# Kernel optimization log

Hardware: AMD Instinct MI355X
Metric: run time of the kernel (lower is better)

Reference implementation:

```python
import jax, jax.numpy as jnp
import numpy as np

D = 128; H = 8; L = 3; FF = 512; HID = 512
B = 512; N = 20
KD = D // H
CLIP = 10.0


def _bn(x, g, b):
    # BatchNorm1d over flattened (B*n, D), training-mode batch stats, affine
    m = jnp.mean(x, axis=(0, 1)); v = jnp.var(x, axis=(0, 1))
    return (x - m) * jax.lax.rsqrt(v + 1e-5) * g + b


def _mha(x, Wq, Wk, Wv, Wo):
    q = jnp.einsum('bnd,hdk->hbnk', x, Wq)
    k = jnp.einsum('bnd,hdk->hbnk', x, Wk)
    v = jnp.einsum('bnd,hdk->hbnk', x, Wv)
    a = jax.nn.softmax(jnp.einsum('hbnk,hbmk->hbnm', q, k) / np.float32(np.sqrt(KD)), axis=-1)
    h = jnp.einsum('hbnm,hbmk->hbnk', a, v)
    return jnp.einsum('hbnk,hkd->bnd', h, Wo)


def _encode(x, Wq, Wk, Wv, Wo, g1, b1, fW1, fb1, fW2, fb2, g2, b2):
    for l in range(L):
        x = _bn(x + _mha(x, Wq[l], Wk[l], Wv[l], Wo[l]), g1[l], b1[l])
        f = jnp.maximum(x @ fW1[l] + fb1[l], 0.0) @ fW2[l] + fb2[l]
        x = _bn(x + f, g2[l], b2[l])
    return x


def _forward(coords, Wi, bi, W_ph, enc_Wq, enc_Wk, enc_Wv, enc_Wo, enc_g1, enc_b1,
             enc_ffW1, enc_ffb1, enc_ffW2, enc_ffb2, enc_g2, enc_b2,
             W_node, W_fixed, W_step, W_out, Wc1, bc1, Wc2, bc2):
    Bs, Ns, _ = coords.shape
    bid = jnp.arange(Bs)
    x = coords @ Wi + bi                                   # (B,N,D) initial embeddings
    crd = coords
    node_idx = jnp.broadcast_to(jnp.arange(Ns)[None, :], (Bs, Ns))
    # state is re-made each step, so step context is always the placeholder
    step_ctx = jnp.broadcast_to(W_ph[None, :], (Bs, 2 * D))
    ctx_q = step_ctx @ W_step                              # (B,D), constant across steps
    log_ps = []; irs = []; vals = []; tours = []
    first = prev = cur = None
    for i in range(Ns):  # sequential decode loop (shapes shrink each step)
        n = Ns - i
        E = _encode(x, enc_Wq, enc_Wk, enc_Wv, enc_Wo, enc_g1, enc_b1,
                    enc_ffW1, enc_ffb1, enc_ffW2, enc_ffb2, enc_g2, enc_b2)  # (B,n,D)
        g_mean = jnp.mean(E, axis=1)                       # (B,D)
        q = g_mean @ W_fixed + ctx_q                       # (B,D)
        gK, gV, lK = jnp.split(E @ W_node, 3, axis=-1)     # each (B,n,D)
        qh = q.reshape(Bs, H, KD)
        a = jax.nn.softmax(jnp.einsum('bhk,bnhk->bhn', qh, gK.reshape(Bs, n, H, KD)) / np.float32(np.sqrt(KD)), axis=-1)
        glimpse = jnp.einsum('bhn,bnhk->bhk', a, gV.reshape(Bs, n, H, KD)).reshape(Bs, D) @ W_out
        logits = jnp.tanh(jnp.einsum('bd,bnd->bn', glimpse, lK) / np.float32(np.sqrt(D))) * CLIP
        log_p = jax.nn.log_softmax(logits, axis=-1)        # mask all-False (fresh state)
        sel = jnp.argmax(log_p, axis=1)                    # greedy decode
        log_ps.append(log_p[bid, sel])
        cur = crd[bid, sel]
        if i == 0:
            first = cur
            irs.append(jnp.zeros((Bs,), coords.dtype))
        else:
            irs.append(-jnp.sqrt(jnp.sum((cur - prev) ** 2, axis=1)))
        h = jnp.maximum(jnp.concatenate([g_mean, step_ctx], axis=1) @ Wc1 + bc1, 0.0)
        vals.append((h @ Wc2 + bc2)[:, 0])
        tours.append(node_idx[bid, sel])
        if i < Ns - 1:
            sel_mask = (jnp.arange(n)[None, :] == sel[:, None]).astype(jnp.int32)
            keep = jnp.argsort(sel_mask, axis=1)[:, : n - 1]  # stable: drops selected, keeps order
            crd = jnp.take_along_axis(crd, keep[:, :, None], axis=1)
            x = jnp.take_along_axis(x, keep[:, :, None], axis=1)
            node_idx = jnp.take_along_axis(node_idx, keep, axis=1)
        prev = cur
    reward_final = -jnp.sqrt(jnp.sum((first - cur) ** 2, axis=1))
    tours = jnp.stack(tours, axis=1)                        # (B,N) int
    d = jnp.take_along_axis(coords, tours[:, :, None], axis=1)
    cost = jnp.sum(jnp.linalg.norm(d[:, 1:] - d[:, :-1], axis=2), axis=1) + jnp.linalg.norm(d[:, 0] - d[:, -1], axis=1)
    return (jnp.stack(log_ps, 1), jnp.stack(irs, 1), jnp.stack(vals, 1), cost, reward_final, tours)


def setup_inputs():
    key = jax.random.key(0)
    ks = jax.random.split(key, 16)
    def nrm(k, shp, scale=0.02):
        return jax.random.normal(k, shp, dtype=jnp.float32) * scale
    return {
        'coords': jax.random.uniform(ks[0], (B, N, 2), dtype=jnp.float32),
        'Wi': nrm(ks[1], (2, D), 0.5),
        'bi': jnp.zeros((D,), jnp.float32),
        'W_ph': jax.random.uniform(ks[2], (2 * D,), jnp.float32, -1.0, 1.0),
        'enc_Wq': nrm(ks[3], (L, H, D, KD)),
        'enc_Wk': nrm(ks[4], (L, H, D, KD)),
        'enc_Wv': nrm(ks[5], (L, H, D, KD)),
        'enc_Wo': nrm(ks[6], (L, H, KD, D)),
        'enc_g1': jnp.ones((L, D), jnp.float32),
        'enc_b1': jnp.zeros((L, D), jnp.float32),
        'enc_ffW1': nrm(ks[7], (L, D, FF)),
        'enc_ffb1': jnp.zeros((L, FF), jnp.float32),
        'enc_ffW2': nrm(ks[8], (L, FF, D)),
        'enc_ffb2': jnp.zeros((L, D), jnp.float32),
        'enc_g2': jnp.ones((L, D), jnp.float32),
        'enc_b2': jnp.zeros((L, D), jnp.float32),
        'W_node': nrm(ks[9], (D, 3 * D)),
        'W_fixed': nrm(ks[10], (D, D)),
        'W_step': nrm(ks[11], (2 * D, D)),
        'W_out': nrm(ks[12], (D, D)),
        'Wc1': nrm(ks[13], (3 * D, HID)),
        'bc1': jnp.zeros((HID,), jnp.float32),
        'Wc2': nrm(ks[14], (HID, 1)),
        'bc2': jnp.zeros((1,), jnp.float32),
    }


def reference(coords, Wi, bi, W_ph, enc_Wq, enc_Wk, enc_Wv, enc_Wo, enc_g1, enc_b1,
              enc_ffW1, enc_ffb1, enc_ffW2, enc_ffb2, enc_g2, enc_b2,
              W_node, W_fixed, W_step, W_out, Wc1, bc1, Wc2, bc2):
    return _forward(coords, Wi, bi, W_ph, enc_Wq, enc_Wk, enc_Wv, enc_Wo, enc_g1, enc_b1,
                    enc_ffW1, enc_ffb1, enc_ffW2, enc_ffb2, enc_g2, enc_b2,
                    W_node, W_fixed, W_step, W_out, Wc1, bc1, Wc2, bc2)
```

## Files before the change

kernel.cpp:

```cpp
#include <hip/hip_runtime.h>
#include <cmath>

namespace {
constexpr int Hc = 8, FFc = 512, HIDc = 512;
}

struct Params {
  const float *coords, *Wi, *bi, *W_ph;
  const float *Wq, *Wk, *Wv, *Wo, *g1, *b1, *fW1, *fb1, *fW2, *fb2, *g2, *b2;
  const float *W_node, *W_fixed, *W_step, *W_out, *Wc1, *bc1, *Wc2, *bc2;
  float* out;
};

__device__ __align__(16) float g_bn[120 * 8 * 256];
__device__ __align__(16) float g_x[512 * 2560];
__device__ __align__(16) float g_t[512 * 2560];
__device__ __align__(16) float g_crd[512 * 40];
__device__ int   g_idx[512 * 20];
__device__ float g_state[512 * 8];
__device__ __align__(16) float g_ctxq[128];
__device__ __align__(16) float g_cctx[512];
__device__ __align__(16) float g_Wqp[3 * 16384];
__device__ __align__(16) float g_Wkp[3 * 16384];
__device__ __align__(16) float g_Wvp[3 * 16384];
__device__ __align__(16) float g_Wop[3 * 16384];
__device__ __align__(16) float g_W1q[3 * 65536];
__device__ __align__(16) float g_W2q[3 * 65536];
__device__ __align__(16) float g_Wnp[49152];
__device__ __align__(16) float g_Wfp[16384];
__device__ __align__(16) float g_Woup[16384];
__device__ __align__(16) float g_Wc1p[65536];

#define DOT4(a, b) ((a).x*(b).x + (a).y*(b).y + (a).z*(b).z + (a).w*(b).w)

__device__ __forceinline__ void bn_coef(int slot, const float* g, const float* bb, float cnt,
                                        float* s_scale, float* s_shift, int tid) {
  if (tid < 128) {
    float sm = 0.f, sq = 0.f;
#pragma unroll
    for (int r = 0; r < 8; r++) {
      const float* s = &g_bn[(slot * 8 + r) * 256];
      sm += s[tid]; sq += s[128 + tid];
    }
    float m_ = sm / cnt;
    float v_ = sq / cnt - m_ * m_;
    float rs = rsqrtf(v_ + 1e-5f);
    float sc = rs * g[tid];
    s_scale[tid] = sc;
    s_shift[tid] = bb[tid] - m_ * sc;
  }
}

__global__ __launch_bounds__(256) void kinit(Params p) {
  const int tid = threadIdx.x, b = blockIdx.x;
  const int gid = b * 256 + tid, GS = 512 * 256;
  for (int i = gid; i < 120 * 8 * 256; i += GS) g_bn[i] = 0.f;
  for (int e = tid; e < 2560; e += 256) {
    int i = e >> 7, d = e & 127;
    float cx = p.coords[b * 40 + 2 * i], cy = p.coords[b * 40 + 2 * i + 1];
    g_x[b * 2560 + e] = cx * p.Wi[d] + cy * p.Wi[128 + d] + p.bi[d];
  }
  if (tid < 40) g_crd[b * 40 + tid] = p.coords[b * 40 + tid];
  if (tid < 20) g_idx[b * 20 + tid] = tid;
  if (tid < 8) g_state[b * 8 + tid] = 0.f;
  if (b == 0) {
    if (tid < 128) {
      float a = 0.f;
      for (int j = 0; j < 256; j++) a += p.W_ph[j] * p.W_step[j * 128 + tid];
      g_ctxq[tid] = a;
    }
    for (int jj = tid; jj < 512; jj += 256) {
      float a = p.bc1[jj];
      for (int e = 0; e < 256; e++) a += p.W_ph[e] * p.Wc1[(128 + e) * 512 + jj];
      g_cctx[jj] = a;
    }
  }
  for (int e = gid; e < 3 * 16384; e += GS) {
    int sub = e & 3, rest = e >> 2;
    int j = rest & 127, rest2 = rest >> 7, d4 = rest2 & 31, l = rest2 >> 5;
    int d = d4 * 4 + sub;
    int src = l * 16384 + (j >> 4) * 2048 + d * 16 + (j & 15);
    g_Wqp[e] = p.Wq[src]; g_Wkp[e] = p.Wk[src]; g_Wvp[e] = p.Wv[src];
    int c = d;
    g_Wop[e] = p.Wo[l * 16384 + (c >> 4) * 2048 + (c & 15) * 128 + j];
  }
  for (int e = gid; e < 3 * 65536; e += GS) {
    int sub = e & 3, f = (e >> 2) & 16383, l = e >> 16;
    int cg = f & 127, c = (f >> 7) & 3, k4 = f >> 9;
    g_W1q[e] = p.fW1[l * 65536 + (k4 * 4 + sub) * 512 + cg * 4 + c];
  }
  for (int e = gid; e < 3 * 65536; e += GS) {
    int sub = e & 3, f = (e >> 2) & 16383, l = e >> 16;
    int j = f & 127, k4 = f >> 7;
    g_W2q[e] = p.fW2[l * 65536 + (k4 * 4 + sub) * 128 + j];
  }
  for (int e = gid; e < 49152; e += GS) {
    int sub = e & 3, rest = e >> 2;
    int col = rest % 384, e4 = rest / 384;
    g_Wnp[e] = p.W_node[(e4 * 4 + sub) * 384 + col];
  }
  for (int e = gid; e < 16384; e += GS) {
    int sub = e & 3, rest = e >> 2;
    int j = rest & 127, e4 = rest >> 7;
    g_Wfp[e] = p.W_fixed[(e4 * 4 + sub) * 128 + j];
    g_Woup[e] = p.W_out[(e4 * 4 + sub) * 128 + j];
  }
  for (int e = gid; e < 65536; e += GS) {
    int sub = e & 3, rest = e >> 2;
    int jj = rest & 511, e4 = rest >> 9;
    g_Wc1p[e] = p.Wc1[(e4 * 4 + sub) * 512 + jj];
  }
}

__global__ __launch_bounds__(512, 4) void ka(Params p, int step, int l) {
  const int tid = threadIdx.x, b = blockIdx.x;
  const int n = 20 - step;
  __shared__ __align__(16) float s_t[2560];
  __shared__ __align__(16) float s_q[2560];
  __shared__ float s_kT[2560];
  __shared__ __align__(16) float s_v[2560];
  __shared__ float s_att[3200];
  __shared__ __align__(16) float s_scale[128], s_shift[128];
  __shared__ float s_bnp[4 * 128 * 2];

  if (l > 0)
    bn_coef(step * 6 + (l - 1) * 2 + 1, p.g2 + (l - 1) * 128, p.b2 + (l - 1) * 128,
            (float)(512 * n), s_scale, s_shift, tid);
  __syncthreads();
  const float4* src4 = (const float4*)((l == 0 ? g_x : g_t) + b * 2560);
  float4* st4 = (float4*)s_t;
  for (int e4 = tid; e4 < n * 32; e4 += 512) {
    float4 x = src4[e4];
    if (l > 0) {
      float4 sc = ((const float4*)s_scale)[e4 & 31];
      float4 sh = ((const float4*)s_shift)[e4 & 31];
      x.x = x.x * sc.x + sh.x; x.y = x.y * sc.y + sh.y;
      x.z = x.z * sc.z + sh.z; x.w = x.w * sc.w + sh.w;
    }
    st4[e4] = x;
  }
  __syncthreads();
  {
    const int j = tid & 127, rg2 = tid >> 7;
    const float4* wq4 = (const float4*)g_Wqp + l * 4096 + j;
    const float4* wk4 = (const float4*)g_Wkp + l * 4096 + j;
    const float4* wv4 = (const float4*)g_Wvp + l * 4096 + j;
    float aq[5], ak[5], av[5];
#pragma unroll
    for (int r = 0; r < 5; r++) { aq[r] = 0.f; ak[r] = 0.f; av[r] = 0.f; }
    float4 bq = wq4[0], bk = wk4[0], bv = wv4[0];
#pragma unroll 2
    for (int d4 = 0; d4 < 32; d4++) {
      const int dn = (d4 + 1) & 31;
      float4 nq = wq4[dn * 128], nk = wk4[dn * 128], nv = wv4[dn * 128];
#pragma unroll
      for (int r = 0; r < 5; r++) {
        int i = rg2 + 4 * r;
        if (i < n) {
          float4 x = st4[i * 32 + d4];
          aq[r] += DOT4(x, bq); ak[r] += DOT4(x, bk); av[r] += DOT4(x, bv);
        }
      }
      bq = nq; bk = nk; bv = nv;
    }
#pragma unroll
    for (int r = 0; r < 5; r++) {
      int i = rg2 + 4 * r;
      if (i < n) {
        s_q[i * 128 + j] = aq[r];
        s_kT[j * 20 + i] = ak[r];
        s_v[i * 128 + j] = av[r];
      }
    }
  }
  __syncthreads();
  const int nn = n * n;
  for (int e = tid; e < 8 * nn; e += 512) {
    int hl = e / nn, rem = e % nn, i = rem / n, m = rem % n;
    float dacc = 0.f;
#pragma unroll
    for (int k2 = 0; k2 < 16; k2++)
      dacc += s_q[i * 128 + hl * 16 + k2] * s_kT[(hl * 16 + k2) * 20 + m];
    s_att[hl * 400 + i * 20 + m] = dacc * 0.25f;
  }
  __syncthreads();
  for (int r = tid; r < 8 * n; r += 512) {
    int hl = r / n, i = r % n;
    float* row = s_att + hl * 400 + i * 20;
    float mx = row[0];
    for (int m = 1; m < n; m++) mx = fmaxf(mx, row[m]);
    float s = 0.f;
    for (int m = 0; m < n; m++) { float ev = __expf(row[m] - mx); row[m] = ev; s += ev; }
    float inv = 1.f / s;
    for (int m = 0; m < n; m++) row[m] *= inv;
  }
  __syncthreads();
  for (int e = tid; e < 8 * n * 16; e += 512) {
    int hl = e / (n * 16), rem = e % (n * 16), i = rem >> 4, k2 = rem & 15;
    const float* arow = s_att + hl * 400 + i * 20;
    float acc = 0.f;
    for (int m = 0; m < n; m++) acc += arow[m] * s_v[m * 128 + hl * 16 + k2];
    s_q[i * 128 + hl * 16 + k2] = acc;
  }
  __syncthreads();
  {
    const int j2 = tid & 127, rh2 = tid >> 7;
    const int s = rh2 & 1, rhalf = rh2 >> 1;
    const float4* sh4 = (const float4*)s_q;
    float acc[5];
#pragma unroll
    for (int r = 0; r < 5; r++) {
      int i = s + 2 * (rhalf + 2 * r);
      acc[r] = (i < n) ? s_t[i * 128 + j2] : 0.f;
    }
    const float4* wo4 = (const float4*)g_Wop + l * 4096 + j2;
    float4 wb0 = wo4[0], wb1 = wo4[128];
#pragma unroll 2
    for (int c4 = 0; c4 < 32; c4++) {
      float4 wn = wo4[((c4 + 2) & 31) * 128];
#pragma unroll
      for (int r = 0; r < 5; r++) {
        int i = s + 2 * (rhalf + 2 * r);
        if (i < n) { float4 h = sh4[i * 32 + c4]; acc[r] += DOT4(h, wb0); }
      }
      wb0 = wb1; wb1 = wn;
    }
    float sm = 0.f, sq = 0.f;
#pragma unroll
    for (int r = 0; r < 5; r++) {
      int i = s + 2 * (rhalf + 2 * r);
      if (i < n) { g_t[b * 2560 + i * 128 + j2] = acc[r]; sm += acc[r]; sq += acc[r] * acc[r]; }
    }
    s_bnp[(rh2 * 128 + j2) * 2] = sm;
    s_bnp[(rh2 * 128 + j2) * 2 + 1] = sq;
  }
  __syncthreads();
  if (tid < 128) {
    float sm = 0.f, sq = 0.f;
#pragma unroll
    for (int h = 0; h < 4; h++) { sm += s_bnp[(h * 128 + tid) * 2]; sq += s_bnp[(h * 128 + tid) * 2 + 1]; }
    float* slot = &g_bn[((step * 6 + l * 2) * 8 + (b & 7)) * 256];
    atomicAdd(&slot[tid], sm);
    atomicAdd(&slot[128 + tid], sq);
  }
}

__global__ __launch_bounds__(256, 4) void kff(Params p, int step, int l) {
  const int tid = threadIdx.x, bx = blockIdx.x;
  const int n = 20 - step;
  const int r0 = bx * 16;
  const int wid = tid >> 6, lam = tid & 63;
  const int g = wid >> 1, rh = wid & 1;
  __shared__ __align__(16) float s_x[16 * 128];
  __shared__ __align__(16) float s_hid[16 * 512];
  __shared__ __align__(16) float s_scale[128], s_shift[128];
  __shared__ float s_bn[8 * 128 * 2];

  bn_coef(step * 6 + l * 2, p.g1 + l * 128, p.b1 + l * 128, (float)(512 * n), s_scale, s_shift, tid);
  __syncthreads();
  {
    float4* sx4 = (float4*)s_x;
    for (int e4 = tid; e4 < 16 * 32; e4 += 256) {
      int row = e4 >> 5, d4 = e4 & 31;
      int r = r0 + row, b = r / n, i = r - b * n;
      float4 x = *(const float4*)(g_t + b * 2560 + i * 128 + d4 * 4);
      float4 sc = ((const float4*)s_scale)[d4];
      float4 sf = ((const float4*)s_shift)[d4];
      x.x = x.x * sc.x + sf.x; x.y = x.y * sc.y + sf.y;
      x.z = x.z * sc.z + sf.z; x.w = x.w * sc.w + sf.w;
      sx4[e4] = x;
    }
  }
  __syncthreads();
  {
    const int cg = g * 64 + lam;
    float acc[8][4];
#pragma unroll
    for (int rr = 0; rr < 8; rr++)
#pragma unroll
      for (int c = 0; c < 4; c++) acc[rr][c] = 0.f;
    const float4* w1 = (const float4*)g_W1q + l * 16384 + cg;
    const float4* xx = (const float4*)s_x + rh * 8 * 32;
    float4 wb[4];
#pragma unroll
    for (int c = 0; c < 4; c++) wb[c] = w1[c * 128];
#pragma unroll 2
    for (int k4 = 0; k4 < 32; k4++) {
      float4 wn[4];
      const int kn = (k4 + 1) & 31;
#pragma unroll
      for (int c = 0; c < 4; c++) wn[c] = w1[kn * 512 + c * 128];
#pragma unroll
      for (int rr = 0; rr < 8; rr++) {
        float4 xr = xx[rr * 32 + k4];
#pragma unroll
        for (int c = 0; c < 4; c++) acc[rr][c] += DOT4(xr, wb[c]);
      }
#pragma unroll
      for (int c = 0; c < 4; c++) wb[c] = wn[c];
    }
    float4 b1v = *(const float4*)(p.fb1 + l * FFc + cg * 4);
#pragma unroll
    for (int rr = 0; rr < 8; rr++) {
      int row = rh * 8 + rr;
      float4 u;
      u.x = fmaxf(acc[rr][0] + b1v.x, 0.f); u.y = fmaxf(acc[rr][1] + b1v.y, 0.f);
      u.z = fmaxf(acc[rr][2] + b1v.z, 0.f); u.w = fmaxf(acc[rr][3] + b1v.w, 0.f);
      *(float4*)&s_hid[row * 512 + cg * 4] = u;
    }
  }
  __syncthreads();
  {
    const int j = g * 64 + lam;
    float acc[8];
#pragma unroll
    for (int rr = 0; rr < 8; rr++) acc[rr] = 0.f;
    const float4* w2 = (const float4*)g_W2q + l * 16384 + j;
    const float4* hh = (const float4*)s_hid + rh * 8 * 128;
    float4 wb0 = w2[0], wb1 = w2[128];
#pragma unroll 2
    for (int k4 = 0; k4 < 128; k4++) {
      float4 wn = w2[((k4 + 2) & 127) * 128];
#pragma unroll
      for (int rr = 0; rr < 8; rr++) acc[rr] += DOT4(hh[rr * 128 + k4], wb0);
      wb0 = wb1; wb1 = wn;
    }
    const float f2 = p.fb2[l * 128 + j];
    float u[8];
#pragma unroll
    for (int rr = 0; rr < 8; rr++) {
      int row = rh * 8 + rr;
      int r = r0 + row, b = r / n, i = r - b * n;
      u[rr] = s_x[row * 128 + j] + acc[rr] + f2;
      g_t[b * 2560 + i * 128 + j] = u[rr];
    }
#pragma unroll
    for (int q = 0; q < 4; q++) {
      const int sb = ((rh * 4 + q) * 128 + j) * 2;
      s_bn[sb] = u[2 * q] + u[2 * q + 1];
      s_bn[sb + 1] = u[2 * q] * u[2 * q] + u[2 * q + 1] * u[2 * q + 1];
    }
  }
  __syncthreads();
  if (tid < 128) {
    float sm = 0.f, sq = 0.f;
#pragma unroll
    for (int rg = 0; rg < 8; rg++) { sm += s_bn[(rg * 128 + tid) * 2]; sq += s_bn[(rg * 128 + tid) * 2 + 1]; }
    float* slot = &g_bn[((step * 6 + l * 2 + 1) * 8 + (bx & 7)) * 256];
    atomicAdd(&slot[tid], sm);
    atomicAdd(&slot[128 + tid], sq);
  }
}

__global__ __launch_bounds__(512, 4) void kd(Params p, int step) {
  const int tid = threadIdx.x, b = blockIdx.x;
  const int n = 20 - step;
  __shared__ __align__(16) float s_t[2560];
  __shared__ __align__(16) float s_dec[7680];
  __shared__ __align__(16) float s_scale[128], s_shift[128];
  __shared__ __align__(16) float s_gmean[128];
  __shared__ float s_red[512];
  __shared__ float s_qv[128], s_glq[128];
  __shared__ __align__(16) float s_gl[128];
  __shared__ float s_att[160];
  __shared__ float s_logits[20];
  __shared__ int s_sel;

  bn_coef(step * 6 + 5, p.g2 + 2 * 128, p.b2 + 2 * 128, (float)(512 * n), s_scale, s_shift, tid);
  __syncthreads();
  const float4* src4 = (const float4*)(g_t + b * 2560);
  float4* st4 = (float4*)s_t;
  for (int e4 = tid; e4 < n * 32; e4 += 512) {
    float4 x = src4[e4];
    float4 sc = ((const float4*)s_scale)[e4 & 31];
    float4 sf = ((const float4*)s_shift)[e4 & 31];
    x.x = x.x * sc.x + sf.x; x.y = x.y * sc.y + sf.y;
    x.z = x.z * sc.z + sf.z; x.w = x.w * sc.w + sf.w;
    st4[e4] = x;
  }
  __syncthreads();
  if (tid < 128) {
    float ssum = 0.f;
    for (int i2 = 0; i2 < n; i2++) ssum += s_t[i2 * 128 + tid];
    s_gmean[tid] = ssum / (float)n;
  }
  __syncthreads();
  {
    const int cb = tid & 63, rg = tid >> 6;
    float acc[6][3];
#pragma unroll
    for (int cc = 0; cc < 6; cc++)
#pragma unroll
      for (int r = 0; r < 3; r++) acc[cc][r] = 0.f;
    const float4* wn4 = (const float4*)g_Wnp + cb;
    float4 wb[6];
#pragma unroll
    for (int cc = 0; cc < 6; cc++) wb[cc] = wn4[cc * 64];
#pragma unroll 2
    for (int d4 = 0; d4 < 32; d4++) {
      const int dn = (d4 + 1) & 31;
      float4 wn[6];
#pragma unroll
      for (int cc = 0; cc < 6; cc++) wn[cc] = wn4[dn * 384 + cc * 64];
#pragma unroll
      for (int r = 0; r < 3; r++) {
        int i = rg + 8 * r;
        if (i < n) {
          float4 x = st4[i * 32 + d4];
#pragma unroll
          for (int cc = 0; cc < 6; cc++) acc[cc][r] += DOT4(x, wb[cc]);
        }
      }
#pragma unroll
      for (int cc = 0; cc < 6; cc++) wb[cc] = wn[cc];
    }
#pragma unroll
    for (int r = 0; r < 3; r++) {
      int i = rg + 8 * r;
      if (i < n) {
#pragma unroll
        for (int cc = 0; cc < 6; cc++)
          s_dec[i * 384 + cb + 64 * cc] = acc[cc][r];
      }
    }
  }
  {
    const int jj = tid;
    float a = g_cctx[jj];
    const float4* wc4 = (const float4*)g_Wc1p + jj;
    const float4* gm4 = (const float4*)s_gmean;
    float4 wb0 = wc4[0], wb1 = wc4[512];
#pragma unroll 2
    for (int e4 = 0; e4 < 32; e4++) {
      float4 wn = wc4[((e4 + 2) & 31) * 512];
      float4 g = gm4[e4]; a += DOT4(g, wb0);
      wb0 = wb1; wb1 = wn;
    }
    s_red[tid] = fmaxf(a, 0.f) * p.Wc2[jj];
  }
  if (tid < 128) {
    float a = g_ctxq[tid];
    const float4* wf4 = (const float4*)g_Wfp + tid;
    const float4* gm4 = (const float4*)s_gmean;
    float4 wb0 = wf4[0], wb1 = wf4[128];
#pragma unroll 2
    for (int e4 = 0; e4 < 32; e4++) {
      float4 wn = wf4[((e4 + 2) & 31) * 128];
      float4 g = gm4[e4]; a += DOT4(g, wb0);
      wb0 = wb1; wb1 = wn;
    }
    s_qv[tid] = a;
  }
  __syncthreads();
#pragma unroll
  for (int sred = 256; sred > 0; sred >>= 1) {
    if (tid < sred) s_red[tid] += s_red[tid + sred];
    __syncthreads();
  }
  for (int e = tid; e < Hc * n; e += 512) {
    int hh = e / n, m = e % n;
    float dacc = 0.f;
#pragma unroll
    for (int k2 = 0; k2 < 16; k2++) dacc += s_qv[hh * 16 + k2] * s_dec[m * 384 + hh * 16 + k2];
    s_att[hh * 20 + m] = dacc * 0.25f;
  }
  __syncthreads();
  if (tid < Hc) {
    float* row = s_att + tid * 20;
    float mx = row[0];
    for (int m = 1; m < n; m++) mx = fmaxf(mx, row[m]);
    float s = 0.f;
    for (int m = 0; m < n; m++) { float ev = __expf(row[m] - mx); row[m] = ev; s += ev; }
    float inv = 1.f / s;
    for (int m = 0; m < n; m++) row[m] *= inv;
  }
  __syncthreads();
  if (tid < 128) {
    int hh = tid >> 4;
    const float* arow = s_att + hh * 20;
    float acc = 0.f;
    for (int m = 0; m < n; m++) acc += arow[m] * s_dec[m * 384 + 128 + tid];
    s_gl[tid] = acc;
  }
  __syncthreads();
  if (tid < 128) {
    float a = 0.f;
    const float4* wo4 = (const float4*)g_Woup + tid;
    const float4* rr4 = (const float4*)s_gl;
    float4 wb0 = wo4[0], wb1 = wo4[128];
#pragma unroll 2
    for (int c4 = 0; c4 < 32; c4++) {
      float4 wn = wo4[((c4 + 2) & 31) * 128];
      float4 r = rr4[c4]; a += DOT4(r, wb0);
      wb0 = wb1; wb1 = wn;
    }
    s_glq[tid] = a;
  }
  __syncthreads();
  if (tid < n) {
    const float* lk = s_dec + tid * 384 + 256;
    float dacc = 0.f;
    for (int d = 0; d < 128; d++) dacc += s_glq[d] * lk[d];
    s_logits[tid] = 10.f * tanhf(dacc / 11.313708498984761f);
  }
  __syncthreads();
  if (tid == 0) {
    float mx = s_logits[0]; int sel = 0;
    for (int i2 = 1; i2 < n; i2++) if (s_logits[i2] > mx) { mx = s_logits[i2]; sel = i2; }
    float s = 0.f;
    for (int i2 = 0; i2 < n; i2++) s += __expf(s_logits[i2] - mx);
    p.out[b * 20 + step] = -logf(s);
    float cx = g_crd[b * 40 + 2 * sel], cy = g_crd[b * 40 + 2 * sel + 1];
    float ir = 0.f;
    if (step > 0) {
      float dx = cx - g_state[b * 8 + 0], dy = cy - g_state[b * 8 + 1];
      float dist = sqrtf(dx * dx + dy * dy);
      ir = -dist;
      g_state[b * 8 + 4] += dist;
    } else { g_state[b * 8 + 2] = cx; g_state[b * 8 + 3] = cy; g_state[b * 8 + 4] = 0.f; }
    p.out[10240 + b * 20 + step] = ir;
    p.out[31744 + b * 20 + step] = (float)g_idx[b * 20 + sel];
    g_state[b * 8 + 0] = cx; g_state[b * 8 + 1] = cy;
    if (step == 19) {
      float dx = g_state[b * 8 + 2] - cx, dy = g_state[b * 8 + 3] - cy;
      float dc = sqrtf(dx * dx + dy * dy);
      p.out[31232 + b] = -dc;
      p.out[30720 + b] = g_state[b * 8 + 4] + dc;
    }
    p.out[20480 + b * 20 + step] = s_red[0] + p.bc2[0];
    s_sel = sel;
  }
  __syncthreads();
  if (step < 19) {
    const int sel = s_sel;
    const int movecnt = (n - 1 - sel) * 128;
    float tmp[5]; float crdv = 0.f; int idxv = 0;
#pragma unroll
    for (int r = 0; r < 5; r++) { int e = tid + r * 512; if (e < movecnt) tmp[r] = g_x[b * 2560 + (sel + 1) * 128 + e]; }
    const int mc2 = (n - 1 - sel) * 2;
    if (tid < mc2) crdv = g_crd[b * 40 + (sel + 1) * 2 + tid];
    if (tid < n - 1 - sel) idxv = g_idx[b * 20 + sel + 1 + tid];
    __syncthreads();
#pragma unroll
    for (int r = 0; r < 5; r++) { int e = tid + r * 512; if (e < movecnt) g_x[b * 2560 + sel * 128 + e] = tmp[r]; }
    if (tid < mc2) g_crd[b * 40 + sel * 2 + tid] = crdv;
    if (tid < n - 1 - sel) g_idx[b * 20 + sel + tid] = idxv;
  }
}

extern "C" void kernel_launch(void* const* d_in, const int* in_sizes, int n_in,
                              void* d_out, int out_size, void* d_ws, size_t ws_size,
                              hipStream_t stream) {
  Params p;
  p.coords  = (const float*)d_in[0];
  p.Wi      = (const float*)d_in[1];
  p.bi      = (const float*)d_in[2];
  p.W_ph    = (const float*)d_in[3];
  p.Wq      = (const float*)d_in[4];
  p.Wk      = (const float*)d_in[5];
  p.Wv      = (const float*)d_in[6];
  p.Wo      = (const float*)d_in[7];
  p.g1      = (const float*)d_in[8];
  p.b1      = (const float*)d_in[9];
  p.fW1     = (const float*)d_in[10];
  p.fb1     = (const float*)d_in[11];
  p.fW2     = (const float*)d_in[12];
  p.fb2     = (const float*)d_in[13];
  p.g2      = (const float*)d_in[14];
  p.b2      = (const float*)d_in[15];
  p.W_node  = (const float*)d_in[16];
  p.W_fixed = (const float*)d_in[17];
  p.W_step  = (const float*)d_in[18];
  p.W_out   = (const float*)d_in[19];
  p.Wc1     = (const float*)d_in[20];
  p.bc1     = (const float*)d_in[21];
  p.Wc2     = (const float*)d_in[22];
  p.bc2     = (const float*)d_in[23];
  p.out = (float*)d_out;

  kinit<<<512, 256, 0, stream>>>(p);
  for (int step = 0; step < 20; step++) {
    const int n = 20 - step;
    for (int l = 0; l < 3; l++) {
      ka<<<512, 512, 0, stream>>>(p, step, l);
      kff<<<dim3(32 * n), 256, 0, stream>>>(p, step, l);
    }
    kd<<<512, 512, 0, stream>>>(p, step);
  }
}
```

Baseline: 5.679 ms.

## Rebalance thread-to-output mapping in attention QKV, FFN and decoder projections

After: 6.268 ms. 10.4% more time.

```diff
diff --git a/kernel.cpp b/kernel.cpp
--- a/kernel.cpp
+++ b/kernel.cpp
@@ -86,8 +86,8 @@
   }
   for (int e = gid; e < 3 * 65536; e += GS) {
     int sub = e & 3, f = (e >> 2) & 16383, l = e >> 16;
-    int cg = f & 127, c = (f >> 7) & 3, k4 = f >> 9;
-    g_W1q[e] = p.fW1[l * 65536 + (k4 * 4 + sub) * 512 + cg * 4 + c];
+    int cg = f & 255, c = (f >> 8) & 1, k4 = f >> 9;
+    g_W1q[e] = p.fW1[l * 65536 + (k4 * 4 + sub) * 512 + cg * 2 + c];
   }
   for (int e = gid; e < 3 * 65536; e += GS) {
     int sub = e & 3, f = (e >> 2) & 16383, l = e >> 16;
@@ -140,22 +140,22 @@
     st4[e4] = x;
   }
   __syncthreads();
-  {
-    const int j = tid & 127, rg2 = tid >> 7;
+  if (tid < 256) {
+    const int j = tid & 127, rg = tid >> 7;
     const float4* wq4 = (const float4*)g_Wqp + l * 4096 + j;
     const float4* wk4 = (const float4*)g_Wkp + l * 4096 + j;
     const float4* wv4 = (const float4*)g_Wvp + l * 4096 + j;
-    float aq[5], ak[5], av[5];
-#pragma unroll
-    for (int r = 0; r < 5; r++) { aq[r] = 0.f; ak[r] = 0.f; av[r] = 0.f; }
+    float aq[10], ak[10], av[10];
+#pragma unroll
+    for (int r = 0; r < 10; r++) { aq[r] = 0.f; ak[r] = 0.f; av[r] = 0.f; }
     float4 bq = wq4[0], bk = wk4[0], bv = wv4[0];
 #pragma unroll 2
     for (int d4 = 0; d4 < 32; d4++) {
       const int dn = (d4 + 1) & 31;
       float4 nq = wq4[dn * 128], nk = wk4[dn * 128], nv = wv4[dn * 128];
 #pragma unroll
-      for (int r = 0; r < 5; r++) {
-        int i = rg2 + 4 * r;
+      for (int r = 0; r < 10; r++) {
+        int i = rg + 2 * r;
         if (i < n) {
           float4 x = st4[i * 32 + d4];
           aq[r] += DOT4(x, bq); ak[r] += DOT4(x, bk); av[r] += DOT4(x, bv);
@@ -164,8 +164,8 @@
       bq = nq; bk = nk; bv = nv;
     }
 #pragma unroll
-    for (int r = 0; r < 5; r++) {
-      int i = rg2 + 4 * r;
+    for (int r = 0; r < 10; r++) {
+      int i = rg + 2 * r;
       if (i < n) {
         s_q[i * 128 + j] = aq[r];
         s_kT[j * 20 + i] = ak[r];
@@ -250,7 +250,6 @@
   const int n = 20 - step;
   const int r0 = bx * 16;
   const int wid = tid >> 6, lam = tid & 63;
-  const int g = wid >> 1, rh = wid & 1;
   __shared__ __align__(16) float s_x[16 * 128];
   __shared__ __align__(16) float s_hid[16 * 512];
   __shared__ __align__(16) float s_scale[128], s_shift[128];
@@ -273,72 +272,79 @@
   }
   __syncthreads();
   {
-    const int cg = g * 64 + lam;
-    float acc[8][4];
-#pragma unroll
-    for (int rr = 0; rr < 8; rr++)
-#pragma unroll
-      for (int c = 0; c < 4; c++) acc[rr][c] = 0.f;
+    const int cg = wid * 64 + lam;
+    float acc[16][2];
+#pragma unroll
+    for (int row = 0; row < 16; row++) { acc[row][0] = 0.f; acc[row][1] = 0.f; }
     const float4* w1 = (const float4*)g_W1q + l * 16384 + cg;
-    const float4* xx = (const float4*)s_x + rh * 8 * 32;
-    float4 wb[4];
-#pragma unroll
-    for (int c = 0; c < 4; c++) wb[c] = w1[c * 128];
+    const float4* xx = (const float4*)s_x;
+    float4 wb0 = w1[0], wb1 = w1[256];
 #pragma unroll 2
     for (int k4 = 0; k4 < 32; k4++) {
-      float4 wn[4];
       const int kn = (k4 + 1) & 31;
-#pragma unroll
-      for (int c = 0; c < 4; c++) wn[c] = w1[kn * 512 + c * 128];
-#pragma unroll
-      for (int rr = 0; rr < 8; rr++) {
-        float4 xr = xx[rr * 32 + k4];
-#pragma unroll
-        for (int c = 0; c < 4; c++) acc[rr][c] += DOT4(xr, wb[c]);
-      }
-#pragma unroll
-      for (int c = 0; c < 4; c++) wb[c] = wn[c];
-    }
-    float4 b1v = *(const float4*)(p.fb1 + l * FFc + cg * 4);
-#pragma unroll
-    for (int rr = 0; rr < 8; rr++) {
-      int row = rh * 8 + rr;
-      float4 u;
-      u.x = fmaxf(acc[rr][0] + b1v.x, 0.f); u.y = fmaxf(acc[rr][1] + b1v.y, 0.f);
-      u.z = fmaxf(acc[rr][2] + b1v.z, 0.f); u.w = fmaxf(acc[rr][3] + b1v.w, 0.f);
-      *(float4*)&s_hid[row * 512 + cg * 4] = u;
+      float4 n0 = w1[kn * 512], n1 = w1[kn * 512 + 256];
+#pragma unroll
+      for (int row = 0; row < 16; row++) {
+        float4 xr = xx[row * 32 + k4];
+        acc[row][0] += DOT4(xr, wb0);
+        acc[row][1] += DOT4(xr, wb1);
+      }
+      wb0 = n0; wb1 = n1;
+    }
+    const float b0 = p.fb1[l * FFc + cg * 2];
+    const float b1 = p.fb1[l * FFc + cg * 2 + 1];
+#pragma unroll
+    for (int row = 0; row < 16; row++) {
+      float2 u;
+      u.x = fmaxf(acc[row][0] + b0, 0.f);
+      u.y = fmaxf(acc[row][1] + b1, 0.f);
+      *(float2*)&s_hid[row * 512 + cg * 2] = u;
     }
   }
   __syncthreads();
   {
-    const int j = g * 64 + lam;
-    float acc[8];
-#pragma unroll
-    for (int rr = 0; rr < 8; rr++) acc[rr] = 0.f;
+    const int kh = wid >> 1, jh = wid & 1, j = jh * 64 + lam;
+    float acc[16];
+#pragma unroll
+    for (int row = 0; row < 16; row++) acc[row] = 0.f;
     const float4* w2 = (const float4*)g_W2q + l * 16384 + j;
-    const float4* hh = (const float4*)s_hid + rh * 8 * 128;
-    float4 wb0 = w2[0], wb1 = w2[128];
-#pragma unroll 2
-    for (int k4 = 0; k4 < 128; k4++) {
-      float4 wn = w2[((k4 + 2) & 127) * 128];
-#pragma unroll
-      for (int rr = 0; rr < 8; rr++) acc[rr] += DOT4(hh[rr * 128 + k4], wb0);
+    const float4* hh = (const float4*)s_hid;
+    const int kbase = kh * 64;
+    float4 wb0 = w2[kbase * 128], wb1 = w2[(kbase + 1) * 128];
+#pragma unroll 2
+    for (int t = 0; t < 64; t++) {
+      const int k4 = kbase + t;
+      const int knt = kbase + ((t + 2) & 63);
+      float4 wn = w2[knt * 128];
+#pragma unroll
+      for (int row = 0; row < 16; row++) acc[row] += DOT4(hh[row * 128 + k4], wb0);
       wb0 = wb1; wb1 = wn;
     }
-    const float f2 = p.fb2[l * 128 + j];
-    float u[8];
-#pragma unroll
-    for (int rr = 0; rr < 8; rr++) {
-      int row = rh * 8 + rr;
-      int r = r0 + row, b = r / n, i = r - b * n;
-      u[rr] = s_x[row * 128 + j] + acc[rr] + f2;
-      g_t[b * 2560 + i * 128 + j] = u[rr];
-    }
-#pragma unroll
-    for (int q = 0; q < 4; q++) {
-      const int sb = ((rh * 4 + q) * 128 + j) * 2;
-      s_bn[sb] = u[2 * q] + u[2 * q + 1];
-      s_bn[sb + 1] = u[2 * q] * u[2 * q] + u[2 * q + 1] * u[2 * q + 1];
+    if (kh == 1) {
+#pragma unroll
+      for (int row = 0; row < 16; row++) s_bn[j * 16 + row] = acc[row];
+    }
+    __syncthreads();
+    float u[16];
+    if (kh == 0) {
+      const float f2 = p.fb2[l * 128 + j];
+#pragma unroll
+      for (int row = 0; row < 16; row++)
+        u[row] = s_x[row * 128 + j] + (acc[row] + s_bn[j * 16 + row]) + f2;
+    }
+    __syncthreads();
+    if (kh == 0) {
+#pragma unroll
+      for (int row = 0; row < 16; row++) {
+        int r = r0 + row, b = r / n, i = r - b * n;
+        g_t[b * 2560 + i * 128 + j] = u[row];
+      }
+#pragma unroll
+      for (int q = 0; q < 8; q++) {
+        const int sb = (q * 128 + j) * 2;
+        s_bn[sb] = u[2 * q] + u[2 * q + 1];
+        s_bn[sb + 1] = u[2 * q] * u[2 * q] + u[2 * q + 1] * u[2 * q + 1];
+      }
     }
   }
   __syncthreads();
@@ -386,41 +392,35 @@
   }
   __syncthreads();
   {
-    const int cb = tid & 63, rg = tid >> 6;
-    float acc[6][3];
-#pragma unroll
-    for (int cc = 0; cc < 6; cc++)
-#pragma unroll
-      for (int r = 0; r < 3; r++) acc[cc][r] = 0.f;
+    const int cb = tid & 127, rg = tid >> 7;
+    float acc[3][5];
+#pragma unroll
+    for (int cc = 0; cc < 3; cc++)
+#pragma unroll
+      for (int r = 0; r < 5; r++) acc[cc][r] = 0.f;
     const float4* wn4 = (const float4*)g_Wnp + cb;
-    float4 wb[6];
-#pragma unroll
-    for (int cc = 0; cc < 6; cc++) wb[cc] = wn4[cc * 64];
+    float4 b0 = wn4[0], b1 = wn4[128], b2 = wn4[256];
 #pragma unroll 2
     for (int d4 = 0; d4 < 32; d4++) {
       const int dn = (d4 + 1) & 31;
-      float4 wn[6];
-#pragma unroll
-      for (int cc = 0; cc < 6; cc++) wn[cc] = wn4[dn * 384 + cc * 64];
-#pragma unroll
-      for (int r = 0; r < 3; r++) {
-        int i = rg + 8 * r;
+      float4 n0 = wn4[dn * 384], n1 = wn4[dn * 384 + 128], n2 = wn4[dn * 384 + 256];
+#pragma unroll
+      for (int r = 0; r < 5; r++) {
+        int i = rg + 4 * r;
         if (i < n) {
           float4 x = st4[i * 32 + d4];
-#pragma unroll
-          for (int cc = 0; cc < 6; cc++) acc[cc][r] += DOT4(x, wb[cc]);
+          acc[0][r] += DOT4(x, b0); acc[1][r] += DOT4(x, b1); acc[2][r] += DOT4(x, b2);
         }
       }
-#pragma unroll
-      for (int cc = 0; cc < 6; cc++) wb[cc] = wn[cc];
-    }
-#pragma unroll
-    for (int r = 0; r < 3; r++) {
-      int i = rg + 8 * r;
+      b0 = n0; b1 = n1; b2 = n2;
+    }
+#pragma unroll
+    for (int r = 0; r < 5; r++) {
+      int i = rg + 4 * r;
       if (i < n) {
 #pragma unroll
-        for (int cc = 0; cc < 6; cc++)
-          s_dec[i * 384 + cb + 64 * cc] = acc[cc][r];
+        for (int cc = 0; cc < 3; cc++)
+          s_dec[i * 384 + cb + 128 * cc] = acc[cc][r];
       }
     }
   }
```
